# Kernel optimization log

Hardware: AMD Instinct MI355X
Metric: run time of the kernel (lower is better)

Reference implementation:

```python
import jax, jax.numpy as jnp
import numpy as np

B, N, C, HEADS, SR = 4, 16384, 64, 2, 8
SIDE = 128            # sqrt(N)
NKV = (SIDE // SR) ** 2  # 256
D = C // HEADS
LN_EPS = 1e-5


def setup_inputs() -> dict:
    key = jax.random.key(0)
    ks = jax.random.split(key, 12)
    s = 0.02
    return {
        "x": jax.random.normal(ks[0], (B, N, C), jnp.float32),
        "pos_2D": jax.random.uniform(ks[1], (B, HEADS, N, NKV), jnp.float32),
        "q_w": jax.random.normal(ks[2], (C, C), jnp.float32) * s,
        "q_b": jnp.zeros((C,), jnp.float32),
        "kv_w": jax.random.normal(ks[3], (2 * C, C), jnp.float32) * s,
        "kv_b": jnp.zeros((2 * C,), jnp.float32),
        "proj_w": jax.random.normal(ks[4], (C, C), jnp.float32) * s,
        "proj_b": jnp.zeros((C,), jnp.float32),
        "sr_w": jax.random.normal(ks[5], (C, C, SR, SR), jnp.float32) * s,  # OIHW
        "sr_b": jnp.zeros((C,), jnp.float32),
        "ln_g": jnp.ones((C,), jnp.float32),
        "ln_b": jnp.zeros((C,), jnp.float32),
        "alpha": jnp.full((1,), 0.3, jnp.float32),
    }


def reference(x, pos_2D, q_w, q_b, kv_w, kv_b, proj_w, proj_b, sr_w, sr_b, ln_g, ln_b, alpha):
    scale = D ** -0.5
    # q projection -> [B, HEADS, N, D]
    q = (jnp.einsum("bnc,oc->bno", x, q_w) + q_b).reshape(B, N, HEADS, D).transpose(0, 2, 1, 3)
    # spatial reduction: conv stride SR on [B, C, SIDE, SIDE]
    xs = x.transpose(0, 2, 1).reshape(B, C, SIDE, SIDE)
    xs = jax.lax.conv_general_dilated(
        xs, sr_w, window_strides=(SR, SR), padding="VALID",
        dimension_numbers=("NCHW", "OIHW", "NCHW")) + sr_b[None, :, None, None]
    xs = xs.reshape(B, C, NKV).transpose(0, 2, 1)  # [B, NKV, C]
    # LayerNorm over channels
    mu = jnp.mean(xs, axis=-1, keepdims=True)
    var = jnp.mean(jnp.square(xs - mu), axis=-1, keepdims=True)
    xs = (xs - mu) * jax.lax.rsqrt(var + LN_EPS) * ln_g + ln_b
    # kv projection -> k, v each [B, HEADS, NKV, D]
    kv = (jnp.einsum("bmc,oc->bmo", xs, kv_w) + kv_b).reshape(B, NKV, 2, HEADS, D)
    kv = kv.transpose(2, 0, 3, 1, 4)
    k, v = kv[0], kv[1]
    # attention with post-softmax positional blend
    attn = jax.nn.softmax(jnp.einsum("bhnd,bhmd->bhnm", q, k) * scale, axis=-1)
    a = alpha[0]
    attn = (1.0 - a) * attn + a * pos_2D
    out = jnp.einsum("bhnm,bhmd->bhnd", attn, v)
    out = out.transpose(0, 2, 1, 3).reshape(B, N, C)
    return jnp.einsum("bnc,oc->bno", out, proj_w) + proj_b
```

## Files before the change

### kernel.cpp

```cpp
#include <hip/hip_runtime.h>
#include <cstdint>
#include <cstddef>

#define NN 16384
#define CC 64
#define LN_EPS 1e-5f

typedef __attribute__((ext_vector_type(8))) short short8;
typedef __attribute__((ext_vector_type(4))) float f32x4;
typedef unsigned short ushort_t;
typedef unsigned int uint32;

__device__ __forceinline__ ushort_t f2bf(float f) {
  union { float f; uint32 u; } v; v.f = f;
  return (ushort_t)((v.u + 0x8000u) >> 16);
}
__device__ __forceinline__ uint32 pk2(float a, float b) {
  union { float f; uint32 u; } x, y; x.f = a; y.f = b;
  return ((x.u + 0x8000u) >> 16) | ((y.u + 0x8000u) & 0xffff0000u);
}
__device__ __forceinline__ short8 pk8(float4 a, float4 b) {
  union { short8 s; uint32 u[4]; } r;
  r.u[0] = pk2(a.x, a.y); r.u[1] = pk2(a.z, a.w);
  r.u[2] = pk2(b.x, b.y); r.u[3] = pk2(b.z, b.w);
  return r.s;
}

__global__ __launch_bounds__(256) void qproj_prep_kernel(const float* __restrict__ x,
    const float* __restrict__ q_w, const float* __restrict__ q_b,
    const float* __restrict__ sr_w, ushort_t* __restrict__ q_out, ushort_t* __restrict__ w3) {
  __shared__ __align__(16) ushort_t q_tile[64*64];
  int t = threadIdx.x;
  {
    int e = blockIdx.x*256 + t;
    int kh = e >> 15, rem = e & 32767, o = rem >> 9, kp = rem & 511;
    int kw = kp >> 6, i = kp & 63;
    w3[e] = f2bf(sr_w[o*4096 + i*64 + kh*8 + kw]);
  }
  int w = t >> 6, lane = t & 63;
  int quad = lane >> 4, col = lane & 15;
  const float qscale = 0.17677669529663687f * 1.4426950408889634f;
  short8 bfr[4][2];
  float qb[4];
  #pragma unroll
  for (int ct = 0; ct < 4; ++ct) {
    #pragma unroll
    for (int ksb = 0; ksb < 2; ++ksb) {
      const float* src = &q_w[(ct*16 + col)*64 + ksb*32 + quad*8];
      bfr[ct][ksb] = pk8(*(const float4*)src, *(const float4*)(src + 4));
    }
    qb[ct] = q_b[ct*16 + col];
  }
  int rows0 = blockIdx.x*64;
  int arow = rows0 + w*16 + col;
  const float* xs = &x[(size_t)arow*64];
  short8 af0 = pk8(*(const float4*)&xs[quad*8],      *(const float4*)&xs[quad*8 + 4]);
  short8 af1 = pk8(*(const float4*)&xs[32 + quad*8], *(const float4*)&xs[36 + quad*8]);
  const f32x4 zero = {0.f, 0.f, 0.f, 0.f};
  #pragma unroll
  for (int ct = 0; ct < 4; ++ct) {
    f32x4 acc = __builtin_amdgcn_mfma_f32_16x16x32_bf16(af0, bfr[ct][0], zero, 0, 0, 0);
    acc = __builtin_amdgcn_mfma_f32_16x16x32_bf16(af1, bfr[ct][1], acc, 0, 0, 0);
    #pragma unroll
    for (int r = 0; r < 4; ++r)
      q_tile[(w*16 + quad*4 + r)*64 + ct*16 + col] = f2bf((acc[r] + qb[ct]) * qscale);
  }
  __syncthreads();
  int u = t;
  #pragma unroll
  for (int s = 0; s < 2; ++s, u += 256) {
    int row = u >> 3, seg = u & 7;
    int h2 = seg >> 2, sg = seg & 3;
    uint4 val = *(const uint4*)&q_tile[row*64 + seg*8];
    int gr = rows0 + row;
    int b2 = gr >> 14, n = gr & 16383;
    *(uint4*)&q_out[((size_t)(b2*2 + h2)*NN + n)*32 + sg*8] = val;
  }
}

__global__ __launch_bounds__(256) void conv_kernel(const float* __restrict__ x,
                                                   const ushort_t* __restrict__ w3,
                                                   float* __restrict__ part) {
  __shared__ __align__(16) ushort_t A_lds[32*520];
  __shared__ __align__(16) ushort_t W_lds[64*520];
  int t = threadIdx.x;
  int pt = blockIdx.x >> 3, kc = blockIdx.x & 7;
  {
    const uint4* src = (const uint4*)&w3[kc*32768];
    #pragma unroll
    for (int v = 0; v < 16; ++v) {
      int g = v*256 + t;
      int o = g >> 6, off8 = (g & 63)*8;
      *(uint4*)&W_lds[o*520 + off8] = src[g];
    }
  }
  #pragma unroll
  for (int v = 0; v < 8; ++v) {
    int g = v*256 + t;
    int pl = g >> 6, off8 = (g & 63)*8;
    int p = pt*32 + pl;
    int b = p >> 8, ph = (p >> 4) & 15, pw = p & 15;
    int n0 = (ph*8 + kc)*128 + pw*8;
    const float* src = &x[((size_t)b*NN + n0)*64 + off8];
    *(short8*)&A_lds[pl*520 + off8] = pk8(*(const float4*)src, *(const float4*)(src + 4));
  }
  __syncthreads();
  int w = t >> 6, lane = t & 63, quad = lane >> 4, col = lane & 15;
  int mt = w & 1, nh = w >> 1;
  const ushort_t* Ab = &A_lds[(mt*16 + col)*520 + quad*8];
  const ushort_t* Bb = &W_lds[(nh*32 + col)*520 + quad*8];
  const f32x4 zero = {0.f, 0.f, 0.f, 0.f};
  f32x4 acc0 = zero, acc1 = zero;
  #pragma unroll
  for (int ks = 0; ks < 16; ++ks) {
    short8 af = *(const short8*)(Ab + ks*32);
    short8 b0 = *(const short8*)(Bb + ks*32);
    short8 b1 = *(const short8*)(Bb + 16*520 + ks*32);
    acc0 = __builtin_amdgcn_mfma_f32_16x16x32_bf16(af, b0, acc0, 0, 0, 0);
    acc1 = __builtin_amdgcn_mfma_f32_16x16x32_bf16(af, b1, acc1, 0, 0, 0);
  }
  #pragma unroll
  for (int r = 0; r < 4; ++r) {
    int p = pt*32 + mt*16 + quad*4 + r;
    part[((kc << 10) + p)*64 + nh*32 + col]      = acc0[r];
    part[((kc << 10) + p)*64 + nh*32 + 16 + col] = acc1[r];
  }
}

__global__ __launch_bounds__(256) void lnkv_kernel(const float* __restrict__ part,
    const float* __restrict__ sr_b, const float* __restrict__ ln_g, const float* __restrict__ ln_b,
    const float* __restrict__ kv_w, const float* __restrict__ kv_b,
    ushort_t* __restrict__ k_out, ushort_t* __restrict__ v_out) {
  __shared__ float xsrow[4][64];
  int t = threadIdx.x;
  int w = t >> 6, lane = t & 63;
  float4 wk[16], wv[16];
  #pragma unroll
  for (int c4 = 0; c4 < 16; ++c4) {
    wk[c4] = *(const float4*)&kv_w[lane*64 + c4*4];
    wv[c4] = *(const float4*)&kv_w[(64+lane)*64 + c4*4];
  }
  float kb0 = kv_b[lane], kb1 = kv_b[64+lane];
  float sb = sr_b[lane], lg = ln_g[lane], lb = ln_b[lane];
  int h = lane >> 5, dd = lane & 31;
  for (int i = 0; i < 2; ++i) {
    int row = blockIdx.x*8 + w*2 + i;
    float xc = sb;
    #pragma unroll
    for (int kc = 0; kc < 8; ++kc) xc += part[kc*65536 + row*64 + lane];
    float s = xc;
    #pragma unroll
    for (int m = 1; m < 64; m <<= 1) s += __shfl_xor(s, m);
    float mu = s * (1.0f/64.0f);
    float d0 = xc - mu;
    float vs = d0*d0;
    #pragma unroll
    for (int m = 1; m < 64; m <<= 1) vs += __shfl_xor(vs, m);
    float rs = rsqrtf(vs*(1.0f/64.0f) + LN_EPS);
    xsrow[w][lane] = d0*rs*lg + lb;
    float acc0 = kb0, acc1 = kb1;
    #pragma unroll
    for (int c4 = 0; c4 < 16; ++c4) {
      float4 xv = *(const float4*)&xsrow[w][c4*4];
      acc0 += xv.x*wk[c4].x + xv.y*wk[c4].y + xv.z*wk[c4].z + xv.w*wk[c4].w;
      acc1 += xv.x*wv[c4].x + xv.y*wv[c4].y + xv.z*wv[c4].z + xv.w*wv[c4].w;
    }
    int b = row >> 8, m2 = row & 255;
    int bh = b*2 + h;
    k_out[(bh*256 + m2)*32 + dd] = f2bf(acc0);
    v_out[(bh*32 + dd)*256 + m2] = f2bf(acc1);
  }
}

__global__ __launch_bounds__(256, 2) void attn_kernel(const ushort_t* __restrict__ q_ws,
    const ushort_t* __restrict__ k_ws, const ushort_t* __restrict__ v_ws,
    const float* __restrict__ pos, const float* __restrict__ alpha,
    ushort_t* __restrict__ attnout) {
  __shared__ __align__(16) ushort_t k_lds[256*40];
  __shared__ __align__(16) ushort_t v_lds[32*264];
  __shared__ __align__(16) ushort_t p_lds[4][16*256];
  __shared__ __align__(16) ushort_t o_lds[4][16*32];
  int t = threadIdx.x;
  int bh = blockIdx.x >> 6, blk = blockIdx.x & 63;
  {
    const uint4* ksrc = (const uint4*)(k_ws + bh*8192);
    const uint4* vsrc = (const uint4*)(v_ws + bh*8192);
    uint4* kd = (uint4*)k_lds; uint4* vd = (uint4*)v_lds;
    #pragma unroll
    for (int vv = 0; vv < 4; ++vv) {
      int i = t + vv*256;
      kd[(i >> 2)*5 + (i & 3)] = ksrc[i];
      vd[(i >> 5)*33 + (i & 31)] = vsrc[i];
    }
  }
  __syncthreads();
  int w = t >> 6, lane = t & 63, quad = lane >> 4, col = lane & 15;
  float a = alpha[0];
  float one_minus_a = 1.0f - a;
  const f32x4 zero = {0.f, 0.f, 0.f, 0.f};
  for (int it = 0; it < 4; ++it) {
    int n0 = blk*256 + (it*4 + w)*16;
    float4 p4[16];
    const float* pbase = &pos[((size_t)bh*NN + n0 + col)*256 + quad*8];
    #pragma unroll
    for (int ks = 0; ks < 8; ++ks) {
      p4[ks*2]   = *(const float4*)(pbase + ks*32);
      p4[ks*2+1] = *(const float4*)(pbase + ks*32 + 4);
    }
    short8 qa = *(const short8*)&q_ws[((size_t)bh*NN + n0 + col)*32 + quad*8];
    f32x4 st[16];
    #pragma unroll
    for (int tt = 0; tt < 16; ++tt) {
      short8 kb = *(const short8*)&k_lds[(tt*16 + col)*40 + quad*8];
      st[tt] = __builtin_amdgcn_mfma_f32_16x16x32_bf16(qa, kb, zero, 0, 0, 0);
    }
    #pragma unroll
    for (int r = 0; r < 4; ++r) {
      float sum = 0.f;
      #pragma unroll
      for (int tt = 0; tt < 16; ++tt) {
        float e = __builtin_amdgcn_exp2f(st[tt][r]);
        st[tt][r] = e; sum += e;
      }
      #pragma unroll
      for (int m = 1; m < 16; m <<= 1) sum += __shfl_xor(sum, m);
      float coef = one_minus_a * __builtin_amdgcn_rcpf(sum);
      int row = quad*4 + r;
      #pragma unroll
      for (int tt = 0; tt < 16; ++tt) {
        float av = st[tt][r]*coef;
        int colg = tt*16 + col;
        int u = colg >> 3, within = colg & 7;
        int usw = u ^ (row & 7);
        p_lds[w][row*256 + usw*8 + within] = f2bf(av);
      }
    }
    f32x4 o0 = zero, o1 = zero, e0 = zero, e1 = zero;
    #pragma unroll
    for (int ks = 0; ks < 8; ++ks) {
      short8 pa  = *(const short8*)&p_lds[w][col*256 + (((ks*4 + quad) ^ (col & 7))*8)];
      short8 vb0 = *(const short8*)&v_lds[(col)*264 + ks*32 + quad*8];
      short8 vb1 = *(const short8*)&v_lds[(16 + col)*264 + ks*32 + quad*8];
      short8 pf  = pk8(p4[ks*2], p4[ks*2+1]);
      o0 = __builtin_amdgcn_mfma_f32_16x16x32_bf16(pa, vb0, o0, 0, 0, 0);
      o1 = __builtin_amdgcn_mfma_f32_16x16x32_bf16(pa, vb1, o1, 0, 0, 0);
      e0 = __builtin_amdgcn_mfma_f32_16x16x32_bf16(pf, vb0, e0, 0, 0, 0);
      e1 = __builtin_amdgcn_mfma_f32_16x16x32_bf16(pf, vb1, e1, 0, 0, 0);
    }
    #pragma unroll
    for (int r = 0; r < 4; ++r) {
      int row = quad*4 + r;
      o_lds[w][row*32 + col]      = f2bf(o0[r] + a*e0[r]);
      o_lds[w][row*32 + 16 + col] = f2bf(o1[r] + a*e1[r]);
    }
    int rowu = lane >> 2, seg = lane & 3;
    uint4 val = *(const uint4*)&o_lds[w][rowu*32 + seg*8];
    *(uint4*)&attnout[((size_t)bh*NN + n0 + rowu)*32 + seg*8] = val;
  }
}

__global__ __launch_bounds__(256) void proj_kernel(const ushort_t* __restrict__ attnout,
    const float* __restrict__ proj_w, const float* __restrict__ proj_b, float* __restrict__ out) {
  __shared__ __align__(16) float o_tile[64*68];
  int t = threadIdx.x;
  int w = t >> 6, lane = t & 63;
  int quad = lane >> 4, col = lane & 15;
  short8 bfr[4][2];
  float pb[4];
  #pragma unroll
  for (int ct = 0; ct < 4; ++ct) {
    #pragma unroll
    for (int ksb = 0; ksb < 2; ++ksb) {
      const float* src = &proj_w[(ct*16 + col)*64 + ksb*32 + quad*8];
      bfr[ct][ksb] = pk8(*(const float4*)src, *(const float4*)(src + 4));
    }
    pb[ct] = proj_b[ct*16 + col];
  }
  int rows0 = blockIdx.x*64;
  int arow = rows0 + w*16 + col;
  int b2 = arow >> 14, n = arow & 16383;
  short8 af0 = *(const short8*)&attnout[((size_t)(b2*2)*NN + n)*32 + quad*8];
  short8 af1 = *(const short8*)&attnout[((size_t)(b2*2 + 1)*NN + n)*32 + quad*8];
  const f32x4 zero = {0.f, 0.f, 0.f, 0.f};
  #pragma unroll
  for (int ct = 0; ct < 4; ++ct) {
    f32x4 acc = __builtin_amdgcn_mfma_f32_16x16x32_bf16(af0, bfr[ct][0], zero, 0, 0, 0);
    acc = __builtin_amdgcn_mfma_f32_16x16x32_bf16(af1, bfr[ct][1], acc, 0, 0, 0);
    #pragma unroll
    for (int r = 0; r < 4; ++r)
      o_tile[(w*16 + quad*4 + r)*68 + ct*16 + col] = acc[r] + pb[ct];
  }
  __syncthreads();
  int u = t;
  #pragma unroll
  for (int s = 0; s < 4; ++s, u += 256) {
    int row = u >> 4, c4 = u & 15;
    float4 val = *(const float4*)&o_tile[row*68 + c4*4];
    *(float4*)&out[(size_t)(rows0 + row)*64 + c4*4] = val;
  }
}

extern "C" void kernel_launch(void* const* d_in, const int* in_sizes, int n_in,
                              void* d_out, int out_size, void* d_ws, size_t ws_size,
                              hipStream_t stream) {
  const float* x      = (const float*)d_in[0];
  const float* pos    = (const float*)d_in[1];
  const float* q_w    = (const float*)d_in[2];
  const float* q_b    = (const float*)d_in[3];
  const float* kv_w   = (const float*)d_in[4];
  const float* kv_b   = (const float*)d_in[5];
  const float* proj_w = (const float*)d_in[6];
  const float* proj_b = (const float*)d_in[7];
  const float* sr_w   = (const float*)d_in[8];
  const float* sr_b   = (const float*)d_in[9];
  const float* ln_g   = (const float*)d_in[10];
  const float* ln_b   = (const float*)d_in[11];
  const float* alpha  = (const float*)d_in[12];
  float* out = (float*)d_out;

  char* ws = (char*)d_ws;
  float* part       = (float*)(ws);
  ushort_t* w3      = (ushort_t*)(ws + (2u<<20));
  ushort_t* k_ws    = (ushort_t*)(ws + (3u<<20));
  ushort_t* v_ws    = (ushort_t*)(ws + (3u<<20) + (128u<<10));
  ushort_t* q_ws    = (ushort_t*)(ws + (4u<<20));
  ushort_t* a_ws    = (ushort_t*)(ws + (12u<<20));

  hipLaunchKernelGGL(qproj_prep_kernel, dim3(1024), dim3(256), 0, stream, x, q_w, q_b, sr_w, q_ws, w3);
  hipLaunchKernelGGL(conv_kernel,       dim3(256),  dim3(256), 0, stream, x, w3, part);
  hipLaunchKernelGGL(lnkv_kernel,       dim3(128),  dim3(256), 0, stream, part, sr_b, ln_g, ln_b, kv_w, kv_b, k_ws, v_ws);
  hipLaunchKernelGGL(attn_kernel,       dim3(512),  dim3(256), 0, stream, q_ws, k_ws, v_ws, pos, alpha, a_ws);
  hipLaunchKernelGGL(proj_kernel,       dim3(1024), dim3(256), 0, stream, a_ws, proj_w, proj_b, out);
}
```

Measured before the change: 264.1 us.

## Transpose attention MFMAs so softmax rows are lane-local and defer normalization

Swaps the MFMA operand order for both QK^T and PV so each lane holds one query row's scores. The softmax sum then needs only two cross-lane shuffles instead of four per row, and P is written to LDS as packed 64-bit stores into a padded layout, replacing scalar swizzled stores. Normalization by 1/sum is deferred to the output, which removes the o_lds staging buffer and the extra LDS round trip before the global store. The risk is that the padded LDS layout causes bank conflicts on the P reads, and the output stores become narrower 8-byte writes.

```diff
diff --git a/kernel.cpp b/kernel.cpp
--- a/kernel.cpp
+++ b/kernel.cpp
@@ -178,8 +178,7 @@
     ushort_t* __restrict__ attnout) {
   __shared__ __align__(16) ushort_t k_lds[256*40];
   __shared__ __align__(16) ushort_t v_lds[32*264];
-  __shared__ __align__(16) ushort_t p_lds[4][16*256];
-  __shared__ __align__(16) ushort_t o_lds[4][16*32];
+  __shared__ __align__(16) ushort_t p_lds[4][16*264];
   int t = threadIdx.x;
   int bh = blockIdx.x >> 6, blk = blockIdx.x & 63;
   {
@@ -212,50 +211,44 @@
     #pragma unroll
     for (int tt = 0; tt < 16; ++tt) {
       short8 kb = *(const short8*)&k_lds[(tt*16 + col)*40 + quad*8];
-      st[tt] = __builtin_amdgcn_mfma_f32_16x16x32_bf16(qa, kb, zero, 0, 0, 0);
-    }
-    #pragma unroll
-    for (int r = 0; r < 4; ++r) {
-      float sum = 0.f;
+      st[tt] = __builtin_amdgcn_mfma_f32_16x16x32_bf16(kb, qa, zero, 0, 0, 0);
+    }
+    float sum = 0.f;
+    #pragma unroll
+    for (int tt = 0; tt < 16; ++tt) {
       #pragma unroll
-      for (int tt = 0; tt < 16; ++tt) {
+      for (int r = 0; r < 4; ++r) {
         float e = __builtin_amdgcn_exp2f(st[tt][r]);
         st[tt][r] = e; sum += e;
       }
-      #pragma unroll
-      for (int m = 1; m < 16; m <<= 1) sum += __shfl_xor(sum, m);
-      float coef = one_minus_a * __builtin_amdgcn_rcpf(sum);
-      int row = quad*4 + r;
-      #pragma unroll
-      for (int tt = 0; tt < 16; ++tt) {
-        float av = st[tt][r]*coef;
-        int colg = tt*16 + col;
-        int u = colg >> 3, within = colg & 7;
-        int usw = u ^ (row & 7);
-        p_lds[w][row*256 + usw*8 + within] = f2bf(av);
-      }
+    }
+    sum += __shfl_xor(sum, 16);
+    sum += __shfl_xor(sum, 32);
+    float coef = one_minus_a * __builtin_amdgcn_rcpf(sum);
+    #pragma unroll
+    for (int tt = 0; tt < 16; ++tt) {
+      uint2 val = { pk2(st[tt][0], st[tt][1]), pk2(st[tt][2], st[tt][3]) };
+      *(uint2*)&p_lds[w][col*264 + tt*16 + quad*4] = val;
     }
     f32x4 o0 = zero, o1 = zero, e0 = zero, e1 = zero;
     #pragma unroll
     for (int ks = 0; ks < 8; ++ks) {
-      short8 pa  = *(const short8*)&p_lds[w][col*256 + (((ks*4 + quad) ^ (col & 7))*8)];
+      short8 pa  = *(const short8*)&p_lds[w][col*264 + ks*32 + quad*8];
       short8 vb0 = *(const short8*)&v_lds[(col)*264 + ks*32 + quad*8];
       short8 vb1 = *(const short8*)&v_lds[(16 + col)*264 + ks*32 + quad*8];
       short8 pf  = pk8(p4[ks*2], p4[ks*2+1]);
-      o0 = __builtin_amdgcn_mfma_f32_16x16x32_bf16(pa, vb0, o0, 0, 0, 0);
-      o1 = __builtin_amdgcn_mfma_f32_16x16x32_bf16(pa, vb1, o1, 0, 0, 0);
-      e0 = __builtin_amdgcn_mfma_f32_16x16x32_bf16(pf, vb0, e0, 0, 0, 0);
-      e1 = __builtin_amdgcn_mfma_f32_16x16x32_bf16(pf, vb1, e1, 0, 0, 0);
-    }
-    #pragma unroll
-    for (int r = 0; r < 4; ++r) {
-      int row = quad*4 + r;
-      o_lds[w][row*32 + col]      = f2bf(o0[r] + a*e0[r]);
-      o_lds[w][row*32 + 16 + col] = f2bf(o1[r] + a*e1[r]);
-    }
-    int rowu = lane >> 2, seg = lane & 3;
-    uint4 val = *(const uint4*)&o_lds[w][rowu*32 + seg*8];
-    *(uint4*)&attnout[((size_t)bh*NN + n0 + rowu)*32 + seg*8] = val;
+      o0 = __builtin_amdgcn_mfma_f32_16x16x32_bf16(vb0, pa, o0, 0, 0, 0);
+      o1 = __builtin_amdgcn_mfma_f32_16x16x32_bf16(vb1, pa, o1, 0, 0, 0);
+      e0 = __builtin_amdgcn_mfma_f32_16x16x32_bf16(vb0, pf, e0, 0, 0, 0);
+      e1 = __builtin_amdgcn_mfma_f32_16x16x32_bf16(vb1, pf, e1, 0, 0, 0);
+    }
+    ushort_t* obase = &attnout[((size_t)bh*NN + n0 + col)*32];
+    uint2 v0 = { pk2(coef*o0[0] + a*e0[0], coef*o0[1] + a*e0[1]),
+                 pk2(coef*o0[2] + a*e0[2], coef*o0[3] + a*e0[3]) };
+    uint2 v1 = { pk2(coef*o1[0] + a*e1[0], coef*o1[1] + a*e1[1]),
+                 pk2(coef*o1[2] + a*e1[2], coef*o1[3] + a*e1[3]) };
+    *(uint2*)&obase[quad*4]      = v0;
+    *(uint2*)&obase[16 + quad*4] = v1;
   }
 }
 
```

Result: no change. 261.4 us (-1.0%).
